# Optimization experiments

Measured on AMD Instinct MI355X. Metric: run time of the kernel, lower is better.

## Reference

```python
import jax, jax.numpy as jnp
import numpy as np

B = 8          # batches
NSX = 8        # subdomains per axis
NSY = 8
NSUB = NSX * NSY
GRID = 64      # points per axis per batch -> 64 points per subdomain
N = B * GRID * GRID
HID = 32       # hidden_channels (also v channels)
OUT = 32       # out_channels
TRES = 64      # max points per subdomain (exact here: uniform grid)


def _point_proj(coords, w1, b1, w2, b2, out_ch, in_ch):
    # PointProjection: Linear(2,hid) -> GELU(exact) -> Linear(hid, out*in) -> [P,out,in]
    h = jax.nn.gelu(coords @ w1 + b1, approximate=False)
    k = h @ w2 + b2
    return k.reshape(coords.shape[0], out_ch, in_ch)


def setup_inputs() -> dict:
    key = jax.random.key(0)
    ks = jax.random.split(key, 9)
    # uniform cell-centered point grid per batch in [0,1]^2
    lin = (jnp.arange(GRID, dtype=jnp.float32) + 0.5) / GRID
    X, Y = jnp.meshgrid(lin, lin, indexing='xy')
    coords1 = jnp.stack([X, Y], axis=-1).reshape(-1, 2)
    src_coords = jnp.tile(coords1, (B, 1))                       # [N,2]
    src_batch = jnp.repeat(jnp.arange(B, dtype=jnp.int32), GRID * GRID)
    v = jax.random.normal(ks[0], (N, HID), jnp.float32)

    def lin_w(k, fan_in, shape):
        bound = 1.0 / np.sqrt(fan_in)
        return jax.random.uniform(k, shape, jnp.float32, -bound, bound)

    return {
        'v': v,
        'src_coords': src_coords,
        'src_batch': src_batch,
        'tgt_res': TRES,
        'src_w1': lin_w(ks[1], 2, (2, HID)),
        'src_b1': lin_w(ks[2], 2, (HID,)),
        'src_w2': lin_w(ks[3], HID, (HID, OUT * HID)),
        'src_b2': lin_w(ks[4], HID, (OUT * HID,)),
        'tgt_w1': lin_w(ks[5], 2, (2, HID)),
        'tgt_b1': lin_w(ks[6], 2, (HID,)),
        'tgt_w2': lin_w(ks[7], HID, (HID, OUT * HID)),
        'tgt_b2': lin_w(ks[8], HID, (OUT * HID,)),
    }


def reference(v, src_coords, src_batch, tgt_res,
              src_w1, src_b1, src_w2, src_b2,
              tgt_w1, tgt_b1, tgt_w2, tgt_b2):
    # --- compute_clusters: assign each point to (batch, subdomain) segment ---
    cx = jnp.clip((src_coords[:, 0] * NSX).astype(jnp.int32), 0, NSX - 1)
    cy = jnp.clip((src_coords[:, 1] * NSY).astype(jnp.int32), 0, NSY - 1)
    seg = src_batch * NSUB + cy * NSX + cx                      # [N]
    S = B * NSUB

    # --- reference target grid in [-1/nsx, 1/nsx] x [-1/nsy, 1/nsy] ---
    x = jnp.linspace(-1.0 / NSX, 1.0 / NSX, tgt_res)
    y = jnp.linspace(-1.0 / NSY, 1.0 / NSY, tgt_res)
    TX, TY = jnp.meshgrid(x, y, indexing='xy')
    tgt_coords = jnp.stack([TX, TY], axis=-1).reshape(-1, 2)    # [T,2], T=tgt_res^2

    # --- per-point MLP kernel projections ---
    psi = _point_proj(src_coords, src_w1, src_b1, src_w2, src_b2, OUT, HID)  # [N,OUT,HID]
    phi = _point_proj(tgt_coords, tgt_w1, tgt_b1, tgt_w2, tgt_b2, OUT, HID)  # [T,OUT,HID]

    # --- segment-wise integral: A[s,o,h] = mean_{x in seg s} psi[x,o,h]*v[x,h] ---
    contrib = psi * v[:, None, :]                                # [N,OUT,HID]
    A = jax.ops.segment_sum(contrib, seg, num_segments=S)        # [S,OUT,HID]
    cnt = jax.ops.segment_sum(jnp.ones((v.shape[0],), v.dtype), seg, num_segments=S)
    A = A / jnp.maximum(cnt, 1.0)[:, None, None]

    # --- contract with target kernel on the reference grid ---
    u = jnp.einsum('toh,soh->sto', phi, A)                       # [S,T,OUT]
    u = u.reshape(B, NSUB, tgt_res, tgt_res, OUT)
    return u
```

## Files before the change

### kernel.cpp

```cpp
#include <hip/hip_runtime.h>
#include <hip/hip_bf16.h>

#define HID   32
#define OUT   32
#define T_TOT 4096
#define S_TOT 512

typedef __attribute__((ext_vector_type(8))) short short8;
typedef __attribute__((ext_vector_type(4))) float f32x4;

__device__ __forceinline__ float gelu_exact(float x) {
    return 0.5f * x * (1.0f + erff(x * 0.70710678118654752440f));
}

__device__ __forceinline__ unsigned int f2bf_u(float x) {
    __hip_bfloat16 h = __float2bfloat16(x);
    unsigned short us = *reinterpret_cast<unsigned short*>(&h);
    return (unsigned int)us;
}

__global__ __launch_bounds__(256) void k_tgt_hidden(
    const float* __restrict__ tw1, const float* __restrict__ tb1,
    unsigned int* __restrict__ Gbf ) {
    int t = blockIdx.x * 256 + threadIdx.x;
    if (t >= T_TOT) return;
    int i = t >> 6, j = t & 63;
    const double step = 0.25 / 63.0;
    float x = (float)(-0.125 + (double)j * step);
    float y = (float)(-0.125 + (double)i * step);
    unsigned int pk[16];
#pragma unroll
    for (int c2 = 0; c2 < 16; ++c2) {
        float z0 = fmaf(x, tw1[2 * c2],     fmaf(y, tw1[HID + 2 * c2],     tb1[2 * c2]));
        float z1 = fmaf(x, tw1[2 * c2 + 1], fmaf(y, tw1[HID + 2 * c2 + 1], tb1[2 * c2 + 1]));
        pk[c2] = f2bf_u(gelu_exact(z0)) | (f2bf_u(gelu_exact(z1)) << 16);
    }
    uint4* dst = (uint4*)(Gbf + (size_t)t * 16);
#pragma unroll
    for (int k = 0; k < 4; ++k)
        dst[k] = make_uint4(pk[4 * k], pk[4 * k + 1], pk[4 * k + 2], pk[4 * k + 3]);
}

__global__ __launch_bounds__(256) void k_segment(
    const float* __restrict__ v, const float* __restrict__ coords,
    const float* __restrict__ sw1, const float* __restrict__ sb1,
    const float* __restrict__ sw2, const float* __restrict__ sb2,
    const float* __restrict__ tw2, const float* __restrict__ tb2,
    unsigned short* __restrict__ Pbf, float* __restrict__ qout) {
    const int s = blockIdx.x;
    const int b = s >> 6, cy = (s >> 3) & 7, cx = s & 7;
    const int tid = threadIdx.x;

    __shared__ float Hs[64][HID];
    __shared__ float Vs[64][HID];
    __shared__ float Ms[HID][HID];
    __shared__ float As[OUT][HID];
    __shared__ float Vsum[HID];

    {
        int r = tid >> 2, qq = tid & 3;
        int p = b * 4096 + (cy * 8 + (r >> 3)) * 64 + cx * 8 + (r & 7);
        const f32x4* src = (const f32x4*)(v + (size_t)p * HID + qq * 8);
        f32x4 a0 = src[0], a1 = src[1];
        *(f32x4*)&Vs[r][qq * 8]     = a0;
        *(f32x4*)&Vs[r][qq * 8 + 4] = a1;

        float x = coords[2 * p], y = coords[2 * p + 1];
#pragma unroll
        for (int e = 0; e < 8; ++e) {
            int c = qq * 8 + e;
            float z = fmaf(x, sw1[c], fmaf(y, sw1[HID + c], sb1[c]));
            Hs[r][c] = gelu_exact(z);
        }
    }
    __syncthreads();

    {
        int c = tid >> 3, hq = tid & 7;
        f32x4 acc = {0.f, 0.f, 0.f, 0.f};
#pragma unroll 16
        for (int r = 0; r < 64; ++r) {
            float hv = Hs[r][c];
            f32x4 vv = *(const f32x4*)&Vs[r][hq * 4];
            acc[0] = fmaf(hv, vv[0], acc[0]);
            acc[1] = fmaf(hv, vv[1], acc[1]);
            acc[2] = fmaf(hv, vv[2], acc[2]);
            acc[3] = fmaf(hv, vv[3], acc[3]);
        }
        *(f32x4*)&Ms[c][hq * 4] = acc;
    }
    if (tid < 32) {
        float sum = 0.f;
#pragma unroll 16
        for (int r = 0; r < 64; ++r) sum += Vs[r][tid];
        Vsum[tid] = sum;
    }
    __syncthreads();

    {
        int o = tid >> 3, hq = tid & 7;
        f32x4 acc = {0.f, 0.f, 0.f, 0.f};
#pragma unroll 8
        for (int c = 0; c < HID; ++c) {
            f32x4 w = *(const f32x4*)(sw2 + (size_t)c * 1024 + o * 32 + hq * 4);
            f32x4 m = *(const f32x4*)&Ms[c][hq * 4];
            acc[0] = fmaf(m[0], w[0], acc[0]);
            acc[1] = fmaf(m[1], w[1], acc[1]);
            acc[2] = fmaf(m[2], w[2], acc[2]);
            acc[3] = fmaf(m[3], w[3], acc[3]);
        }
        f32x4 bb = *(const f32x4*)(sb2 + o * 32 + hq * 4);
        f32x4 vs = *(const f32x4*)&Vsum[hq * 4];
        acc[0] = fmaf(bb[0], vs[0], acc[0]);
        acc[1] = fmaf(bb[1], vs[1], acc[1]);
        acc[2] = fmaf(bb[2], vs[2], acc[2]);
        acc[3] = fmaf(bb[3], vs[3], acc[3]);
        const float inv = 1.0f / 64.0f;
        acc[0] *= inv; acc[1] *= inv; acc[2] *= inv; acc[3] *= inv;
        *(f32x4*)&As[o][hq * 4] = acc;
    }
    __syncthreads();

    {
        int o = tid >> 3, cq = tid & 7;
        f32x4 a[8];
#pragma unroll
        for (int hq = 0; hq < 8; ++hq) a[hq] = *(const f32x4*)&As[o][hq * 4];

        unsigned int pk[2];
#pragma unroll
        for (int k2 = 0; k2 < 2; ++k2) {
            unsigned int w01 = 0;
#pragma unroll
            for (int kk = 0; kk < 2; ++kk) {
                int c = cq * 4 + k2 * 2 + kk;
                float acc = 0.f;
#pragma unroll
                for (int hq = 0; hq < 8; ++hq) {
                    f32x4 w = *(const f32x4*)(tw2 + (size_t)c * 1024 + o * 32 + hq * 4);
                    acc = fmaf(w[0], a[hq][0], acc);
                    acc = fmaf(w[1], a[hq][1], acc);
                    acc = fmaf(w[2], a[hq][2], acc);
                    acc = fmaf(w[3], a[hq][3], acc);
                }
                w01 |= f2bf_u(acc) << (16 * kk);
            }
            pk[k2] = w01;
        }
        uint2 val; val.x = pk[0]; val.y = pk[1];
        *(uint2*)(Pbf + (size_t)s * 1024 + o * 32 + cq * 4) = val;

        if (cq == 0) {
            float acc = 0.f;
#pragma unroll
            for (int hq = 0; hq < 8; ++hq) {
                f32x4 tb = *(const f32x4*)(tb2 + o * 32 + hq * 4);
                acc = fmaf(tb[0], a[hq][0], acc);
                acc = fmaf(tb[1], a[hq][1], acc);
                acc = fmaf(tb[2], a[hq][2], acc);
                acc = fmaf(tb[3], a[hq][3], acc);
            }
            qout[s * 32 + o] = acc;
        }
    }
}

__global__ __launch_bounds__(256) void k_contract(
    const unsigned short* __restrict__ Gbf,
    const unsigned short* __restrict__ Pbf,
    const float* __restrict__ q,
    float* __restrict__ u) {
    const int s    = blockIdx.y;
    const int lane = threadIdx.x & 63;
    const int wave = threadIdx.x >> 6;
    const int lo = lane & 15;
    const int lk = lane >> 4;

    const unsigned short* pb = Pbf + (size_t)s * 1024;
    short8 p0 = *(const short8*)(pb + lo * 32 + lk * 8);
    short8 p1 = *(const short8*)(pb + (16 + lo) * 32 + lk * 8);

    f32x4 c0, c1;
#pragma unroll
    for (int j = 0; j < 4; ++j) {
        c0[j] = q[s * 32 + lk * 4 + j];
        c1[j] = q[s * 32 + 16 + lk * 4 + j];
    }

    const int tbase = blockIdx.x * 1024 + wave * 256;
    float* ubase = u + (size_t)s * (T_TOT * 32);

#pragma unroll 4
    for (int tile = 0; tile < 16; ++tile) {
        int t0 = tbase + tile * 16;
        short8 gfrag = *(const short8*)(Gbf + (size_t)(t0 + lo) * 32 + lk * 8);
        f32x4 d0 = __builtin_amdgcn_mfma_f32_16x16x32_bf16(p0, gfrag, c0, 0, 0, 0);
        f32x4 d1 = __builtin_amdgcn_mfma_f32_16x16x32_bf16(p1, gfrag, c1, 0, 0, 0);
        float* up = ubase + (size_t)(t0 + lo) * 32;
        *(f32x4*)(up + lk * 4)      = d0;
        *(f32x4*)(up + 16 + lk * 4) = d1;
    }
}

extern "C" void kernel_launch(void* const* d_in, const int* in_sizes, int n_in,
                              void* d_out, int out_size, void* d_ws, size_t ws_size,
                              hipStream_t stream) {
    (void)in_sizes; (void)n_in; (void)out_size; (void)ws_size;
    const float* v       = (const float*)d_in[0];
    const float* scoords = (const float*)d_in[1];
    const float* sw1 = (const float*)d_in[4];
    const float* sb1 = (const float*)d_in[5];
    const float* sw2 = (const float*)d_in[6];
    const float* sb2 = (const float*)d_in[7];
    const float* tw1 = (const float*)d_in[8];
    const float* tb1 = (const float*)d_in[9];
    const float* tw2 = (const float*)d_in[10];
    const float* tb2 = (const float*)d_in[11];
    float* u = (float*)d_out;

    char* ws = (char*)d_ws;
    unsigned int*   Gbf  = (unsigned int*)ws;
    unsigned short* Pbf  = (unsigned short*)(ws + 262144);
    float*          qbuf = (float*)(ws + 262144 + 1048576);

    hipLaunchKernelGGL(k_tgt_hidden, dim3(16), dim3(256), 0, stream, tw1, tb1, Gbf);
    hipLaunchKernelGGL(k_segment, dim3(S_TOT), dim3(256), 0, stream,
                       v, scoords, sw1, sb1, sw2, sb2, tw2, tb2,
                       Pbf, qbuf);
    hipLaunchKernelGGL(k_contract, dim3(4, S_TOT), dim3(256), 0, stream,
                       (const unsigned short*)Gbf, (const unsigned short*)Pbf, qbuf, u);
}
```

Before: 72.98 us.

## Fuse segment reduction and MFMA contraction into one 1024-thread kernel

Merges the per-segment reduction kernel and the contraction kernel into one kernel with 1024 threads per block. The first 256 threads build the P and q matrices in shared memory, and all 16 waves then run the MFMA contraction over the 4096 targets. This removes the global round trip for P and q and one kernel launch. In exchange, 768 threads sit idle during the reduction phases. The 1024-thread block with launch_bounds(1024,8) may also limit register allocation and occupancy.

```diff
diff --git a/kernel.cpp b/kernel.cpp
--- a/kernel.cpp
+++ b/kernel.cpp
@@ -41,12 +41,13 @@
         dst[k] = make_uint4(pk[4 * k], pk[4 * k + 1], pk[4 * k + 2], pk[4 * k + 3]);
 }
 
-__global__ __launch_bounds__(256) void k_segment(
+__global__ __launch_bounds__(1024, 8) void k_fused(
     const float* __restrict__ v, const float* __restrict__ coords,
     const float* __restrict__ sw1, const float* __restrict__ sb1,
     const float* __restrict__ sw2, const float* __restrict__ sb2,
     const float* __restrict__ tw2, const float* __restrict__ tb2,
-    unsigned short* __restrict__ Pbf, float* __restrict__ qout) {
+    const unsigned short* __restrict__ Gbf,
+    float* __restrict__ u) {
     const int s = blockIdx.x;
     const int b = s >> 6, cy = (s >> 3) & 7, cx = s & 7;
     const int tid = threadIdx.x;
@@ -56,8 +57,10 @@
     __shared__ float Ms[HID][HID];
     __shared__ float As[OUT][HID];
     __shared__ float Vsum[HID];
-
-    {
+    __shared__ float qls[OUT];
+    __shared__ unsigned int Pli[512];
+
+    if (tid < 256) {
         int r = tid >> 2, qq = tid & 3;
         int p = b * 4096 + (cy * 8 + (r >> 3)) * 64 + cx * 8 + (r & 7);
         const f32x4* src = (const f32x4*)(v + (size_t)p * HID + qq * 8);
@@ -75,7 +78,7 @@
     }
     __syncthreads();
 
-    {
+    if (tid < 256) {
         int c = tid >> 3, hq = tid & 7;
         f32x4 acc = {0.f, 0.f, 0.f, 0.f};
 #pragma unroll 16
@@ -97,7 +100,7 @@
     }
     __syncthreads();
 
-    {
+    if (tid < 256) {
         int o = tid >> 3, hq = tid & 7;
         f32x4 acc = {0.f, 0.f, 0.f, 0.f};
 #pragma unroll 8
@@ -121,78 +124,64 @@
     }
     __syncthreads();
 
-    {
+    if (tid < 256) {
         int o = tid >> 3, cq = tid & 7;
-        f32x4 a[8];
-#pragma unroll
-        for (int hq = 0; hq < 8; ++hq) a[hq] = *(const f32x4*)&As[o][hq * 4];
-
-        unsigned int pk[2];
-#pragma unroll
-        for (int k2 = 0; k2 < 2; ++k2) {
-            unsigned int w01 = 0;
-#pragma unroll
-            for (int kk = 0; kk < 2; ++kk) {
-                int c = cq * 4 + k2 * 2 + kk;
-                float acc = 0.f;
-#pragma unroll
-                for (int hq = 0; hq < 8; ++hq) {
-                    f32x4 w = *(const f32x4*)(tw2 + (size_t)c * 1024 + o * 32 + hq * 4);
-                    acc = fmaf(w[0], a[hq][0], acc);
-                    acc = fmaf(w[1], a[hq][1], acc);
-                    acc = fmaf(w[2], a[hq][2], acc);
-                    acc = fmaf(w[3], a[hq][3], acc);
-                }
-                w01 |= f2bf_u(acc) << (16 * kk);
+        float a0 = 0.f, a1 = 0.f, a2 = 0.f, a3 = 0.f, qacc = 0.f;
+#pragma unroll
+        for (int hq = 0; hq < 8; ++hq) {
+            f32x4 a = *(const f32x4*)&As[o][hq * 4];
+#pragma unroll
+            for (int kk = 0; kk < 4; ++kk) {
+                int c = cq * 4 + kk;
+                f32x4 w = *(const f32x4*)(tw2 + (size_t)c * 1024 + o * 32 + hq * 4);
+                float t = fmaf(w[0], a[0], fmaf(w[1], a[1], 0.f));
+                float partial = (kk == 0) ? a0 : (kk == 1) ? a1 : (kk == 2) ? a2 : a3;
+                partial = fmaf(w[0], a[0], partial);
+                partial = fmaf(w[1], a[1], partial);
+                partial = fmaf(w[2], a[2], partial);
+                partial = fmaf(w[3], a[3], partial);
+                if (kk == 0) a0 = partial; else if (kk == 1) a1 = partial;
+                else if (kk == 2) a2 = partial; else a3 = partial;
+                (void)t;
             }
-            pk[k2] = w01;
-        }
-        uint2 val; val.x = pk[0]; val.y = pk[1];
-        *(uint2*)(Pbf + (size_t)s * 1024 + o * 32 + cq * 4) = val;
-
-        if (cq == 0) {
-            float acc = 0.f;
-#pragma unroll
-            for (int hq = 0; hq < 8; ++hq) {
+            if (cq == 0) {
                 f32x4 tb = *(const f32x4*)(tb2 + o * 32 + hq * 4);
-                acc = fmaf(tb[0], a[hq][0], acc);
-                acc = fmaf(tb[1], a[hq][1], acc);
-                acc = fmaf(tb[2], a[hq][2], acc);
-                acc = fmaf(tb[3], a[hq][3], acc);
+                qacc = fmaf(tb[0], a[0], qacc);
+                qacc = fmaf(tb[1], a[1], qacc);
+                qacc = fmaf(tb[2], a[2], qacc);
+                qacc = fmaf(tb[3], a[3], qacc);
             }
-            qout[s * 32 + o] = acc;
-        }
-    }
-}
-
-__global__ __launch_bounds__(256) void k_contract(
-    const unsigned short* __restrict__ Gbf,
-    const unsigned short* __restrict__ Pbf,
-    const float* __restrict__ q,
-    float* __restrict__ u) {
-    const int s    = blockIdx.y;
-    const int lane = threadIdx.x & 63;
-    const int wave = threadIdx.x >> 6;
+        }
+        Pli[o * 16 + cq * 2]     = f2bf_u(a0) | (f2bf_u(a1) << 16);
+        Pli[o * 16 + cq * 2 + 1] = f2bf_u(a2) | (f2bf_u(a3) << 16);
+        if (cq == 0) qls[o] = qacc;
+    }
+    __syncthreads();
+
+    const int lane = tid & 63;
+    const int wave = tid >> 6;
     const int lo = lane & 15;
     const int lk = lane >> 4;
 
-    const unsigned short* pb = Pbf + (size_t)s * 1024;
-    short8 p0 = *(const short8*)(pb + lo * 32 + lk * 8);
-    short8 p1 = *(const short8*)(pb + (16 + lo) * 32 + lk * 8);
+    uint4 pu0 = *(const uint4*)&Pli[lo * 16 + lk * 4];
+    uint4 pu1 = *(const uint4*)&Pli[(16 + lo) * 16 + lk * 4];
+    short8 p0, p1;
+    __builtin_memcpy(&p0, &pu0, 16);
+    __builtin_memcpy(&p1, &pu1, 16);
 
     f32x4 c0, c1;
 #pragma unroll
     for (int j = 0; j < 4; ++j) {
-        c0[j] = q[s * 32 + lk * 4 + j];
-        c1[j] = q[s * 32 + 16 + lk * 4 + j];
-    }
-
-    const int tbase = blockIdx.x * 1024 + wave * 256;
+        c0[j] = qls[lk * 4 + j];
+        c1[j] = qls[16 + lk * 4 + j];
+    }
+
+    const int tw = wave * 256;
     float* ubase = u + (size_t)s * (T_TOT * 32);
 
 #pragma unroll 4
     for (int tile = 0; tile < 16; ++tile) {
-        int t0 = tbase + tile * 16;
+        int t0 = tw + tile * 16;
         short8 gfrag = *(const short8*)(Gbf + (size_t)(t0 + lo) * 32 + lk * 8);
         f32x4 d0 = __builtin_amdgcn_mfma_f32_16x16x32_bf16(p0, gfrag, c0, 0, 0, 0);
         f32x4 d1 = __builtin_amdgcn_mfma_f32_16x16x32_bf16(p1, gfrag, c1, 0, 0, 0);
@@ -218,15 +207,10 @@
     const float* tb2 = (const float*)d_in[11];
     float* u = (float*)d_out;
 
-    char* ws = (char*)d_ws;
-    unsigned int*   Gbf  = (unsigned int*)ws;
-    unsigned short* Pbf  = (unsigned short*)(ws + 262144);
-    float*          qbuf = (float*)(ws + 262144 + 1048576);
+    unsigned int* Gbf = (unsigned int*)d_ws;
 
     hipLaunchKernelGGL(k_tgt_hidden, dim3(16), dim3(256), 0, stream, tw1, tb1, Gbf);
-    hipLaunchKernelGGL(k_segment, dim3(S_TOT), dim3(256), 0, stream,
+    hipLaunchKernelGGL(k_fused, dim3(S_TOT), dim3(1024), 0, stream,
                        v, scoords, sw1, sb1, sw2, sb2, tw2, tb2,
-                       Pbf, qbuf);
-    hipLaunchKernelGGL(k_contract, dim3(4, S_TOT), dim3(256), 0, stream,
-                       (const unsigned short*)Gbf, (const unsigned short*)Pbf, qbuf, u);
-}
+                       (const unsigned short*)Gbf, u);
+}
```

Result: slower. 105.1 us (+44.0%).
